# Performance work log

Hardware: AMD Instinct MI355X
Metric: run time of the kernel (lower is better)

## Reference

```python
import jax, jax.numpy as jnp
import numpy as np

B, S, H, D = 2, 2048, 2048, 256  # batch, seq, hidden, head_dim
NH, NKV = 8, 1                   # attention heads, kv heads
N_REP = NH // NKV
SCALING = D ** -0.5
ROPE_THETA = 10000.0
NEG_INF = -1e9


def rotate_half(x):
    x1, x2 = jnp.split(x, 2, axis=-1)
    return jnp.concatenate((-x2, x1), axis=-1)


def setup_inputs() -> dict:
    key = jax.random.key(0)
    ks = jax.random.split(key, 5)
    hidden_states = jax.random.normal(ks[0], (B, S, H), dtype=jnp.float32)
    # RoPE cos/sin per position, Gemma-style: inv_freq tiled over full head_dim
    inv_freq = 1.0 / (ROPE_THETA ** (np.arange(0, D, 2, dtype=np.float32) / D))  # [D/2]
    pos = np.arange(S, dtype=np.float32)
    freqs = np.outer(pos, inv_freq)                      # [S, D/2]
    emb = np.concatenate([freqs, freqs], axis=-1)        # [S, D]
    cos = jnp.broadcast_to(jnp.asarray(np.cos(emb)), (B, S, D))
    sin = jnp.broadcast_to(jnp.asarray(np.sin(emb)), (B, S, D))
    # additive causal mask [B, 1, S, S]
    causal = jnp.triu(jnp.full((S, S), NEG_INF, dtype=jnp.float32), k=1)
    attention_mask = jnp.broadcast_to(causal[None, None], (B, 1, S, S))
    scale = 0.02
    Wq = jax.random.normal(ks[1], (H, NH * D), dtype=jnp.float32) * scale
    Wk = jax.random.normal(ks[2], (H, NKV * D), dtype=jnp.float32) * scale
    Wv = jax.random.normal(ks[3], (H, NKV * D), dtype=jnp.float32) * scale
    Wo = jax.random.normal(ks[4], (NH * D, H), dtype=jnp.float32) * scale
    return {"hidden_states": hidden_states, "cos": cos, "sin": sin,
            "attention_mask": attention_mask, "Wq": Wq, "Wk": Wk, "Wv": Wv, "Wo": Wo}


def reference(hidden_states, cos, sin, attention_mask, Wq, Wk, Wv, Wo):
    # projections: [B,S,H] @ [H, nh*D] -> [B, nh, S, D]
    q = (hidden_states @ Wq).reshape(B, S, NH, D).transpose(0, 2, 1, 3)
    k = (hidden_states @ Wk).reshape(B, S, NKV, D).transpose(0, 2, 1, 3)
    v = (hidden_states @ Wv).reshape(B, S, NKV, D).transpose(0, 2, 1, 3)
    # RoPE (cos/sin broadcast over head dim via unsqueeze at axis 1)
    c = cos[:, None]  # [B,1,S,D]
    s = sin[:, None]
    q = q * c + rotate_half(q) * s
    k = k * c + rotate_half(k) * s
    # repeat_kv: [B, NKV, S, D] -> [B, NH, S, D]
    k = jnp.repeat(k, N_REP, axis=1)
    v = jnp.repeat(v, N_REP, axis=1)
    # eager attention
    attn_weights = jnp.einsum("bhqd,bhkd->bhqk", q, k) * SCALING
    attn_weights = attn_weights + attention_mask[:, :, :, :S]
    attn_weights = jax.nn.softmax(attn_weights.astype(jnp.float32), axis=-1).astype(q.dtype)
    attn_output = jnp.einsum("bhqk,bhkd->bhqd", attn_weights, v)
    attn_output = attn_output.transpose(0, 2, 1, 3).reshape(B, S, NH * D)
    attn_output = attn_output @ Wo
    return attn_output, attn_weights
```

## Files before the change

### kernel.cpp

```cpp
#include <hip/hip_runtime.h>
#include <hip/hip_bf16.h>

#define B_   2
#define S_   2048
#define H_   2048
#define D_   256
#define NH_  8

typedef unsigned short u16;
typedef __bf16 bf16x8 __attribute__((ext_vector_type(8)));
typedef float f32x4 __attribute__((ext_vector_type(4)));
typedef unsigned int uint4v __attribute__((ext_vector_type(4)));
typedef unsigned int uint2v __attribute__((ext_vector_type(2)));

#define AS1 __attribute__((address_space(1)))
#define AS3 __attribute__((address_space(3)))

__device__ __forceinline__ u16 f2bf(float x) {
  union { float f; unsigned u; } v; v.f = x;
  unsigned u = v.u;
  u += 0x7FFFu + ((u >> 16) & 1u);
  return (u16)(u >> 16);
}
__device__ __forceinline__ float bf2f(u16 x) {
  union { unsigned u; float f; } v; v.u = ((unsigned)x) << 16;
  return v.f;
}

__device__ __forceinline__ void bf8_unpack(uint4v u, float* f) {
  f[0] = bf2f(u.x & 0xffff); f[1] = bf2f(u.x >> 16);
  f[2] = bf2f(u.y & 0xffff); f[3] = bf2f(u.y >> 16);
  f[4] = bf2f(u.z & 0xffff); f[5] = bf2f(u.z >> 16);
  f[6] = bf2f(u.w & 0xffff); f[7] = bf2f(u.w >> 16);
}
__device__ __forceinline__ uint4v bf8_pack(const float* f) {
  uint4v o;
  o.x = (unsigned)f2bf(f[0]) | ((unsigned)f2bf(f[1]) << 16);
  o.y = (unsigned)f2bf(f[2]) | ((unsigned)f2bf(f[3]) << 16);
  o.z = (unsigned)f2bf(f[4]) | ((unsigned)f2bf(f[5]) << 16);
  o.w = (unsigned)f2bf(f[6]) | ((unsigned)f2bf(f[7]) << 16);
  return o;
}

__device__ __forceinline__ void gld_lds16(const u16* g, u16* l) {
  __builtin_amdgcn_global_load_lds((const AS1 unsigned int*)g,
                                   (AS3 unsigned int*)l, 16, 0, 0);
}

#define BM 128
#define BN 128
#define BK 32

enum GemmMode { MODE_PROJ = 0, MODE_QK = 1, MODE_PV = 2, MODE_WO = 3 };

template <int MODE>
__global__ __launch_bounds__(256)
void gemm_nt(const u16* __restrict__ A, const u16* __restrict__ Bb,
             void* __restrict__ Cp, float* __restrict__ rows,
             float* __restrict__ Pout,
             int K, int lda, int ldb, int ldc)
{
  int bn, bm;
  if constexpr (MODE == MODE_QK) {
    int t = blockIdx.x;
    bm = 0;
    while ((bm + 1) * (bm + 2) / 2 <= t) bm++;
    bn = t - bm * (bm + 1) / 2;
  } else if constexpr (MODE == MODE_PV) {
    bn = blockIdx.x;
    bm = (int)gridDim.y - 1 - (int)blockIdx.y;
  } else {
    bn = blockIdx.x;
    bm = blockIdx.y;
  }
  const int bz = blockIdx.z;
  const int m0 = bm * BM, n0 = bn * BN;
  const int tid = threadIdx.x;

  const u16* Ap = A;
  const u16* Bp = Bb;
  float* Cf = (float*)Cp;
  u16*   Cu = (u16*)Cp;
  float* Pp = Pout;

  if constexpr (MODE == MODE_QK) {
    Ap   += (size_t)bz * S_ * D_;
    Bp   += (size_t)(bz >> 3) * S_ * D_;
    Cu   += (size_t)bz * S_ * S_;
    rows += (size_t)bz * S_;
  } else if constexpr (MODE == MODE_PV) {
    Ap   += (size_t)bz * S_ * S_;
    Bp   += (size_t)(bz >> 3) * D_ * S_;
    Cu   += (size_t)(bz >> 3) * S_ * (NH_ * D_) + (size_t)(bz & 7) * D_;
    rows += (size_t)bz * S_;
    Pp   += (size_t)bz * S_ * S_;
  }

  if constexpr (MODE == MODE_PV) {
    if (bn == 2) {
      const int k0 = tid * 8;
      for (int rr = 0; rr < BM; ++rr) {
        const int q = m0 + rr;
        const u16* e = Ap + (size_t)q * S_ + k0;
        float* p = Pp + (size_t)q * S_ + k0;
        const float inv = 1.0f / rows[q];
        float4 lo = {0.f, 0.f, 0.f, 0.f}, hi = {0.f, 0.f, 0.f, 0.f};
        if (k0 <= q) {
          uint4v u = *(const uint4v*)e;
          float v[8];
          bf8_unpack(u, v);
          lo.x = (k0 + 0 <= q) ? v[0] * inv : 0.f;
          lo.y = (k0 + 1 <= q) ? v[1] * inv : 0.f;
          lo.z = (k0 + 2 <= q) ? v[2] * inv : 0.f;
          lo.w = (k0 + 3 <= q) ? v[3] * inv : 0.f;
          hi.x = (k0 + 4 <= q) ? v[4] * inv : 0.f;
          hi.y = (k0 + 5 <= q) ? v[5] * inv : 0.f;
          hi.z = (k0 + 6 <= q) ? v[6] * inv : 0.f;
          hi.w = (k0 + 7 <= q) ? v[7] * inv : 0.f;
        }
        *(float4*)p       = lo;
        *(float4*)(p + 4) = hi;
      }
      return;
    }
  }

  int Keff = K;
  if constexpr (MODE == MODE_PV) {
    int lim = (bm + 1) * BM;
    Keff = lim < K ? lim : K;
  }

  __shared__ __align__(16) u16 smem[BM * BK + BN * BK + 512];
  u16* As = smem;
  u16* Bs = smem + BM * BK;
  __shared__ float invs[BM];

  const int lane = tid & 63;
  const int quad = lane >> 4;
  const int l16  = lane & 15;
  const int wave = tid >> 6;
  const int wm   = (wave >> 1) << 6;
  const int wn   = (wave & 1) << 6;

  if constexpr (MODE == MODE_PV) {
    if (tid < BM) invs[tid] = 1.0f / rows[m0 + tid];
  }

  f32x4 acc[4][4] = {};

  for (int kt = 0; kt < Keff; kt += BK) {
    #pragma unroll
    for (int i = 0; i < 2; i++) {
      int c = tid + i * 256;
      gld_lds16(Ap + (size_t)(m0 + (c >> 2)) * lda + kt + (c & 3) * 8, &As[c * 8]);
    }
    #pragma unroll
    for (int i = 0; i < 2; i++) {
      int c = tid + i * 256;
      gld_lds16(Bp + (size_t)(n0 + (c >> 2)) * ldb + kt + (c & 3) * 8, &Bs[c * 8]);
    }
    __syncthreads();

    bf16x8 af[4], bfr[4];
    #pragma unroll
    for (int i = 0; i < 4; i++)
      af[i] = *(const bf16x8*)(&As[(wm + i * 16 + l16) * BK + quad * 8]);
    #pragma unroll
    for (int j = 0; j < 4; j++)
      bfr[j] = *(const bf16x8*)(&Bs[(wn + j * 16 + l16) * BK + quad * 8]);
    #pragma unroll
    for (int i = 0; i < 4; i++)
      #pragma unroll
      for (int j = 0; j < 4; j++)
        acc[i][j] = __builtin_amdgcn_mfma_f32_16x16x32_bf16(af[i], bfr[j], acc[i][j], 0, 0, 0);
    __syncthreads();
  }

  const float SCL2 = 0.0625f * 1.44269504088896340736f;
  if constexpr (MODE == MODE_WO) {
    float (*Cs32)[132] = (float (*)[132])smem;
    const int band16 = (wave >> 1) * 16;
    #pragma unroll
    for (int i = 0; i < 4; i++) {
      #pragma unroll
      for (int r = 0; r < 4; r++) {
        const int lr = band16 + quad * 4 + r;
        #pragma unroll
        for (int j = 0; j < 4; j++)
          Cs32[lr][wn + j * 16 + l16] = acc[i][j][r];
      }
      __syncthreads();
      #pragma unroll
      for (int ch = tid; ch < 1024; ch += 256) {
        const int rr = ch >> 5, cc = ch & 31;
        const int mg = m0 + ((rr >> 4) << 6) + i * 16 + (rr & 15);
        *(float4*)(Cf + (size_t)mg * ldc + n0 + cc * 4) =
            *(const float4*)(&Cs32[rr][cc * 4]);
      }
      __syncthreads();
    }
  } else {
    u16 (*Cs)[136] = (u16 (*)[136])smem;
    const int band16 = (wave >> 1) * 16;
    #pragma unroll
    for (int i = 0; i < 4; i++) {
      #pragma unroll
      for (int r = 0; r < 4; r++) {
        const int lr = band16 + quad * 4 + r;
        const int m  = m0 + wm + i * 16 + quad * 4 + r;
        if constexpr (MODE == MODE_QK) {
          float rs = 0.f;
          #pragma unroll
          for (int j = 0; j < 4; j++) {
            int n = n0 + wn + j * 16 + l16;
            float e = (n <= m) ? exp2f(acc[i][j][r] * SCL2) : 0.f;
            rs += e;
            Cs[lr][wn + j * 16 + l16] = f2bf(e);
          }
          #pragma unroll
          for (int o = 1; o < 16; o <<= 1) rs += __shfl_xor(rs, o, 64);
          if (l16 == 0) atomicAdd(&rows[m], rs);
        } else if constexpr (MODE == MODE_PV) {
          const float inv = invs[wm + i * 16 + quad * 4 + r];
          #pragma unroll
          for (int j = 0; j < 4; j++)
            Cs[lr][wn + j * 16 + l16] = f2bf(acc[i][j][r] * inv);
        } else {
          #pragma unroll
          for (int j = 0; j < 4; j++)
            Cs[lr][wn + j * 16 + l16] = f2bf(acc[i][j][r]);
        }
      }
      __syncthreads();
      #pragma unroll
      for (int ch = tid; ch < 512; ch += 256) {
        const int rr = ch >> 4, cc = ch & 15;
        const int mg = m0 + ((rr >> 4) << 6) + i * 16 + (rr & 15);
        *(uint4v*)(Cu + (size_t)mg * ldc + n0 + cc * 8) =
            *(const uint4v*)(&Cs[rr][cc * 8]);
      }
      __syncthreads();
    }
  }
}

__device__ __forceinline__ void tc_tile(const float* __restrict__ src,
                                        u16* __restrict__ dst, int K, int N,
                                        int n0, int k0, float (*t)[33])
{
  int c = threadIdx.x & 31, r = threadIdx.x >> 5;
  #pragma unroll
  for (int rr = 0; rr < 32; rr += 8)
    t[r + rr][c] = src[(size_t)(k0 + r + rr) * N + n0 + c];
  __syncthreads();
  #pragma unroll
  for (int rr = 0; rr < 32; rr += 8)
    dst[(size_t)(n0 + r + rr) * K + k0 + c] = f2bf(t[c][r + rr]);
}

__global__ __launch_bounds__(256)
void prep_kernel(const float* __restrict__ X,
                 const float* __restrict__ Wq, const float* __restrict__ Wk,
                 const float* __restrict__ Wv, const float* __restrict__ Wo,
                 u16* __restrict__ Xbf, u16* __restrict__ WT,
                 u16* __restrict__ WoT, float* __restrict__ Rows)
{
  __shared__ float t[32][33];
  const int bid = blockIdx.x;
  if (bid < 4096) {
    tc_tile(Wq, WT, 2048, 2048, (bid & 63) * 32, (bid >> 6) * 32, t);
  } else if (bid < 4608) {
    int l = bid - 4096;
    tc_tile(Wk, WT + 2048 * 2048, 2048, 256, (l & 7) * 32, (l >> 3) * 32, t);
  } else if (bid < 5120) {
    int l = bid - 4608;
    tc_tile(Wv, WT + 2304 * 2048, 2048, 256, (l & 7) * 32, (l >> 3) * 32, t);
  } else if (bid < 9216) {
    int l = bid - 5120;
    tc_tile(Wo, WoT, 2048, 2048, (l & 63) * 32, (l >> 6) * 32, t);
  } else if (bid < 11264) {
    int l = bid - 9216;
    #pragma unroll
    for (int it = 0; it < 4; ++it) {
      int i = it * 524288 + l * 256 + threadIdx.x;
      float4 f = ((const float4*)X)[i];
      uint2v p;
      p.x = (unsigned)f2bf(f.x) | ((unsigned)f2bf(f.y) << 16);
      p.y = (unsigned)f2bf(f.z) | ((unsigned)f2bf(f.w) << 16);
      ((uint2v*)Xbf)[i] = p;
    }
  } else {
    int l = bid - 11264;
    const float4 z = {0.f, 0.f, 0.f, 0.f};
    #pragma unroll
    for (int it = 0; it < 4; ++it)
      ((float4*)Rows)[it * 2048 + l * 256 + threadIdx.x] = z;
  }
}

__global__ __launch_bounds__(256)
void postproj_kernel(const u16* __restrict__ raw, const float* __restrict__ cosb,
                     const float* __restrict__ sinb, u16* __restrict__ qout,
                     u16* __restrict__ kout, u16* __restrict__ vt)
{
  __shared__ u16 t[32][34];
  const int bid = blockIdx.x;
  if (bid < 1024) {
    const int row = threadIdx.x >> 4;
    const int d8  = (threadIdx.x & 15) * 8;
    #pragma unroll
    for (int it2 = 0; it2 < 2; ++it2) {
      int idx = bid * 32 + it2 * 16 + row;
      int h = idx & 7, bs = idx >> 3;
      int b = bs >> 11, s = bs & (S_ - 1);
      size_t base = (size_t)bs * 2560 + (size_t)h * D_;
      uint4v u1 = *(const uint4v*)(raw + base + d8);
      uint4v u2 = *(const uint4v*)(raw + base + 128 + d8);
      float4 c0 = *(const float4*)(cosb + (size_t)bs * D_ + d8);
      float4 c1 = *(const float4*)(cosb + (size_t)bs * D_ + d8 + 4);
      float4 s0 = *(const float4*)(sinb + (size_t)bs * D_ + d8);
      float4 s1 = *(const float4*)(sinb + (size_t)bs * D_ + d8 + 4);
      float a[8], bq[8], cc[8], ss[8], r1[8], r2[8];
      bf8_unpack(u1, a); bf8_unpack(u2, bq);
      cc[0]=c0.x; cc[1]=c0.y; cc[2]=c0.z; cc[3]=c0.w;
      cc[4]=c1.x; cc[5]=c1.y; cc[6]=c1.z; cc[7]=c1.w;
      ss[0]=s0.x; ss[1]=s0.y; ss[2]=s0.z; ss[3]=s0.w;
      ss[4]=s1.x; ss[5]=s1.y; ss[6]=s1.z; ss[7]=s1.w;
      #pragma unroll
      for (int i = 0; i < 8; ++i) {
        r1[i] = a[i] * cc[i] - bq[i] * ss[i];
        r2[i] = bq[i] * cc[i] + a[i] * ss[i];
      }
      size_t ob = (((size_t)b * NH_ + h) * S_ + s) * D_;
      *(uint4v*)(qout + ob + d8)       = bf8_pack(r1);
      *(uint4v*)(qout + ob + 128 + d8) = bf8_pack(r2);
    }
  } else if (bid < 1280) {
    const int l   = bid - 1024;
    const int row = threadIdx.x >> 4;
    const int d8  = (threadIdx.x & 15) * 8;
    int bs = l * 16 + row;
    size_t base = (size_t)bs * 2560 + 2048;
    uint4v u1 = *(const uint4v*)(raw + base + d8);
    uint4v u2 = *(const uint4v*)(raw + base + 128 + d8);
    float4 c0 = *(const float4*)(cosb + (size_t)bs * D_ + d8);
    float4 c1 = *(const float4*)(cosb + (size_t)bs * D_ + d8 + 4);
    float4 s0 = *(const float4*)(sinb + (size_t)bs * D_ + d8);
    float4 s1 = *(const float4*)(sinb + (size_t)bs * D_ + d8 + 4);
    float a[8], bq[8], cc[8], ss[8], r1[8], r2[8];
    bf8_unpack(u1, a); bf8_unpack(u2, bq);
    cc[0]=c0.x; cc[1]=c0.y; cc[2]=c0.z; cc[3]=c0.w;
    cc[4]=c1.x; cc[5]=c1.y; cc[6]=c1.z; cc[7]=c1.w;
    ss[0]=s0.x; ss[1]=s0.y; ss[2]=s0.z; ss[3]=s0.w;
    ss[4]=s1.x; ss[5]=s1.y; ss[6]=s1.z; ss[7]=s1.w;
    #pragma unroll
    for (int i = 0; i < 8; ++i) {
      r1[i] = a[i] * cc[i] - bq[i] * ss[i];
      r2[i] = bq[i] * cc[i] + a[i] * ss[i];
    }
    *(uint4v*)(kout + (size_t)bs * D_ + d8)       = bf8_pack(r1);
    *(uint4v*)(kout + (size_t)bs * D_ + 128 + d8) = bf8_pack(r2);
  } else {
    int l = bid - 1280;
    int b = l >> 9, rem = l & 511;
    int d0 = (rem & 7) * 32, s0 = (rem >> 3) * 32;
    int c = threadIdx.x & 31, r = threadIdx.x >> 5;
    #pragma unroll
    for (int rr = 0; rr < 32; rr += 8)
      t[r + rr][c] = raw[(size_t)(b * S_ + s0 + r + rr) * 2560 + 2304 + d0 + c];
    __syncthreads();
    #pragma unroll
    for (int rr = 0; rr < 32; rr += 8)
      vt[(size_t)b * D_ * S_ + (size_t)(d0 + r + rr) * S_ + s0 + c] = t[c][r + rr];
  }
}

extern "C" void kernel_launch(void* const* d_in, const int* in_sizes, int n_in,
                              void* d_out, int out_size, void* d_ws, size_t ws_size,
                              hipStream_t stream)
{
  const float* X    = (const float*)d_in[0];
  const float* cosb = (const float*)d_in[1];
  const float* sinb = (const float*)d_in[2];
  const float* Wq   = (const float*)d_in[4];
  const float* Wk   = (const float*)d_in[5];
  const float* Wv   = (const float*)d_in[6];
  const float* Wo   = (const float*)d_in[7];

  float* outO = (float*)d_out;
  float* outP = outO + (size_t)B_ * S_ * H_;

  u16* ws     = (u16*)d_ws;
  u16* Xbf    = ws;
  u16* WT     = Xbf    + 8388608;
  u16* WoT    = WT     + 5242880;
  u16* QKVraw = WoT    + 4194304;
  u16* Qbf    = QKVraw + 10485760;
  u16* Kbf    = Qbf    + 8388608;
  u16* VT     = Kbf    + 1048576;
  u16* AObf   = VT     + 1048576;
  u16* Ebf    = AObf   + 8388608;
  float* Rows = (float*)(Ebf + 67108864);

  prep_kernel<<<11272, 256, 0, stream>>>(X, Wq, Wk, Wv, Wo, Xbf, WT, WoT, Rows);
  gemm_nt<MODE_PROJ><<<dim3(20, 32, 1), 256, 0, stream>>>(
      Xbf, WT, QKVraw, nullptr, nullptr, 2048, 2048, 2048, 2560);
  postproj_kernel<<<2304, 256, 0, stream>>>(QKVraw, cosb, sinb, Qbf, Kbf, VT);
  gemm_nt<MODE_QK><<<dim3(136, 1, 16), 256, 0, stream>>>(
      Qbf, Kbf, Ebf, Rows, nullptr, 256, 256, 256, 2048);
  gemm_nt<MODE_PV><<<dim3(3, 16, 16), 256, 0, stream>>>(
      Ebf, VT, AObf, Rows, outP, 2048, 2048, 2048, 2048);
  gemm_nt<MODE_WO><<<dim3(16, 32, 1), 256, 0, stream>>>(
      AObf, WoT, outO, nullptr, nullptr, 2048, 2048, 2048, 2048);
}
```

Before: 662.7 us.

## Double GEMM K-tile and fuse probability write into PV main loop

Raises the K tile from 32 to 64 in all GEMM modes, so each barrier pair now covers two MFMA sub-steps. It also drops the separate third PV block column that reread E from global to write the normalized fp32 probabilities. Instead, the bn==0 block writes probabilities from the E tile already staged in LDS, then zero-fills the masked tail after the loop. This removes a redundant global read of E and a grid column, but doubles LDS use per block and puts the store work on the critical path of one block column.

Result: no change. 665.2 us (+0.4%).

```diff
diff --git a/kernel.cpp b/kernel.cpp
--- a/kernel.cpp
+++ b/kernel.cpp
@@ -49,7 +49,7 @@
 
 #define BM 128
 #define BN 128
-#define BK 32
+#define BK 64
 
 enum GemmMode { MODE_PROJ = 0, MODE_QK = 1, MODE_PV = 2, MODE_WO = 3 };
 
@@ -96,35 +96,6 @@
     Pp   += (size_t)bz * S_ * S_;
   }
 
-  if constexpr (MODE == MODE_PV) {
-    if (bn == 2) {
-      const int k0 = tid * 8;
-      for (int rr = 0; rr < BM; ++rr) {
-        const int q = m0 + rr;
-        const u16* e = Ap + (size_t)q * S_ + k0;
-        float* p = Pp + (size_t)q * S_ + k0;
-        const float inv = 1.0f / rows[q];
-        float4 lo = {0.f, 0.f, 0.f, 0.f}, hi = {0.f, 0.f, 0.f, 0.f};
-        if (k0 <= q) {
-          uint4v u = *(const uint4v*)e;
-          float v[8];
-          bf8_unpack(u, v);
-          lo.x = (k0 + 0 <= q) ? v[0] * inv : 0.f;
-          lo.y = (k0 + 1 <= q) ? v[1] * inv : 0.f;
-          lo.z = (k0 + 2 <= q) ? v[2] * inv : 0.f;
-          lo.w = (k0 + 3 <= q) ? v[3] * inv : 0.f;
-          hi.x = (k0 + 4 <= q) ? v[4] * inv : 0.f;
-          hi.y = (k0 + 5 <= q) ? v[5] * inv : 0.f;
-          hi.z = (k0 + 6 <= q) ? v[6] * inv : 0.f;
-          hi.w = (k0 + 7 <= q) ? v[7] * inv : 0.f;
-        }
-        *(float4*)p       = lo;
-        *(float4*)(p + 4) = hi;
-      }
-      return;
-    }
-  }
-
   int Keff = K;
   if constexpr (MODE == MODE_PV) {
     int lim = (bm + 1) * BM;
@@ -151,30 +122,64 @@
 
   for (int kt = 0; kt < Keff; kt += BK) {
     #pragma unroll
-    for (int i = 0; i < 2; i++) {
+    for (int i = 0; i < 4; i++) {
       int c = tid + i * 256;
-      gld_lds16(Ap + (size_t)(m0 + (c >> 2)) * lda + kt + (c & 3) * 8, &As[c * 8]);
-    }
-    #pragma unroll
-    for (int i = 0; i < 2; i++) {
+      gld_lds16(Ap + (size_t)(m0 + (c >> 3)) * lda + kt + (c & 7) * 8, &As[c * 8]);
+    }
+    #pragma unroll
+    for (int i = 0; i < 4; i++) {
       int c = tid + i * 256;
-      gld_lds16(Bp + (size_t)(n0 + (c >> 2)) * ldb + kt + (c & 3) * 8, &Bs[c * 8]);
+      gld_lds16(Bp + (size_t)(n0 + (c >> 3)) * ldb + kt + (c & 7) * 8, &Bs[c * 8]);
     }
     __syncthreads();
 
-    bf16x8 af[4], bfr[4];
-    #pragma unroll
-    for (int i = 0; i < 4; i++)
-      af[i] = *(const bf16x8*)(&As[(wm + i * 16 + l16) * BK + quad * 8]);
-    #pragma unroll
-    for (int j = 0; j < 4; j++)
-      bfr[j] = *(const bf16x8*)(&Bs[(wn + j * 16 + l16) * BK + quad * 8]);
-    #pragma unroll
-    for (int i = 0; i < 4; i++)
+    #pragma unroll
+    for (int kk = 0; kk < 2; kk++) {
+      bf16x8 af[4], bfr[4];
+      #pragma unroll
+      for (int i = 0; i < 4; i++)
+        af[i] = *(const bf16x8*)(&As[(wm + i * 16 + l16) * BK + kk * 32 + quad * 8]);
       #pragma unroll
       for (int j = 0; j < 4; j++)
-        acc[i][j] = __builtin_amdgcn_mfma_f32_16x16x32_bf16(af[i], bfr[j], acc[i][j], 0, 0, 0);
+        bfr[j] = *(const bf16x8*)(&Bs[(wn + j * 16 + l16) * BK + kk * 32 + quad * 8]);
+      #pragma unroll
+      for (int i = 0; i < 4; i++)
+        #pragma unroll
+        for (int j = 0; j < 4; j++)
+          acc[i][j] = __builtin_amdgcn_mfma_f32_16x16x32_bf16(af[i], bfr[j], acc[i][j], 0, 0, 0);
+    }
+
+    if constexpr (MODE == MODE_PV) {
+      if (bn == 0) {
+        const int pr4 = tid >> 4;
+        const int pc4 = (tid & 15) * 4;
+        #pragma unroll
+        for (int rr = 0; rr < BM; rr += 16) {
+          const int r = rr + pr4;
+          const u16* e = &As[r * BK + pc4];
+          const float inv = invs[r];
+          float4 o;
+          o.x = bf2f(e[0]) * inv; o.y = bf2f(e[1]) * inv;
+          o.z = bf2f(e[2]) * inv; o.w = bf2f(e[3]) * inv;
+          *(float4*)(Pp + (size_t)(m0 + r) * S_ + kt + pc4) = o;
+        }
+      }
+    }
     __syncthreads();
+  }
+
+  if constexpr (MODE == MODE_PV) {
+    if (bn == 0 && Keff < S_) {
+      const int r8 = tid >> 3;
+      const int c8 = tid & 7;
+      const float4 z = {0.f, 0.f, 0.f, 0.f};
+      #pragma unroll
+      for (int rr = 0; rr < BM; rr += 32) {
+        float* pr = Pp + (size_t)(m0 + rr + r8) * S_;
+        for (int c4 = (Keff >> 2) + c8; c4 < (S_ >> 2); c4 += 8)
+          *(float4*)(pr + c4 * 4) = z;
+      }
+    }
   }
 
   const float SCL2 = 0.0625f * 1.44269504088896340736f;
@@ -409,7 +414,7 @@
   postproj_kernel<<<2304, 256, 0, stream>>>(QKVraw, cosb, sinb, Qbf, Kbf, VT);
   gemm_nt<MODE_QK><<<dim3(136, 1, 16), 256, 0, stream>>>(
       Qbf, Kbf, Ebf, Rows, nullptr, 256, 256, 256, 2048);
-  gemm_nt<MODE_PV><<<dim3(3, 16, 16), 256, 0, stream>>>(
+  gemm_nt<MODE_PV><<<dim3(2, 16, 16), 256, 0, stream>>>(
       Ebf, VT, AObf, Rows, outP, 2048, 2048, 2048, 2048);
   gemm_nt<MODE_WO><<<dim3(16, 32, 1), 256, 0, stream>>>(
       AObf, WoT, outO, nullptr, nullptr, 2048, 2048, 2048, 2048);
```
